# Optimization experiments

Measured on AMD Instinct MI355X. Metric: run time of the kernel, lower is better.

The kernel has to match this reference:

```python
import jax, jax.numpy as jnp
import numpy as np

N_NODES = 10000
N_EDGES = 160000
HID = 128
N_LAYERS = 6
N_RBF = 50
CUTOFF = 10.0
EDGE_IN = 2 * HID + N_RBF + 1  # 307


def setup_inputs() -> dict:
    key = jax.random.key(0)
    ks = jax.random.split(key, 24)
    s = 0.05
    inp = {
        'atomic_numbers': jax.random.randint(ks[0], (N_NODES,), 0, 100),
        'coords': jax.random.normal(ks[1], (N_NODES, 3), jnp.float32),
        'edge_index': jax.random.randint(ks[2], (2, N_EDGES), 0, N_NODES),
        'embed': jax.random.normal(ks[3], (100, HID), jnp.float32) * s,
        # message_net (stacked over layers)
        'mw1': jax.random.normal(ks[4], (N_LAYERS, EDGE_IN, HID), jnp.float32) * s,
        'mb1': jnp.zeros((N_LAYERS, HID), jnp.float32),
        'mw2': jax.random.normal(ks[5], (N_LAYERS, HID, HID), jnp.float32) * s,
        'mb2': jnp.zeros((N_LAYERS, HID), jnp.float32),
        # coord_net
        'cw1': jax.random.normal(ks[6], (N_LAYERS, HID, HID), jnp.float32) * s,
        'cb1': jnp.zeros((N_LAYERS, HID), jnp.float32),
        'cw2': jax.random.normal(ks[7], (N_LAYERS, HID, 1), jnp.float32) * s,
        'cb2': jnp.zeros((N_LAYERS, 1), jnp.float32),
        # feature_net
        'fw': jax.random.normal(ks[8], (N_LAYERS, 2 * HID, HID), jnp.float32) * s,
        'fb': jnp.zeros((N_LAYERS, HID), jnp.float32),
        # energy_predictor
        'ew1': jax.random.normal(ks[9], (HID, HID), jnp.float32) * s,
        'eb1': jnp.zeros((HID,), jnp.float32),
        'ew2': jax.random.normal(ks[10], (HID, 1), jnp.float32) * s,
        'eb2': jnp.zeros((1,), jnp.float32),
    }
    return inp


def _forward(atomic_numbers, coords, edge_index, embed,
             mw1, mb1, mw2, mb2, cw1, cb1, cw2, cb2, fw, fb,
             ew1, eb1, ew2, eb2):
    silu = jax.nn.silu
    n = coords.shape[0]
    row, col = edge_index[0], edge_index[1]
    feats = embed[atomic_numbers]                    # [N, H]
    # RBF edge attributes (computed once from initial coords)
    d = jnp.linalg.norm(coords[row] - coords[col], axis=-1)[:, None]  # [E,1]
    centers = jnp.linspace(0.0, CUTOFF, N_RBF)
    width = CUTOFF / N_RBF
    rbf = jnp.exp(-((d - centers) ** 2) / width)
    cut = 0.5 * (jnp.cos(jnp.pi * d / CUTOFF) + 1.0) * (d < CUTOFF).astype(d.dtype)
    edge_attr = rbf * cut                            # [E, 50]
    for l in range(N_LAYERS):
        diff = coords[row] - coords[col]             # [E, 3]
        edist = jnp.sum(diff * diff, axis=-1, keepdims=True)  # squared dist, [E,1]
        ef = jnp.concatenate([feats[row], feats[col], edist, edge_attr], axis=-1)
        m = silu(silu(ef @ mw1[l] + mb1[l]) @ mw2[l] + mb2[l])        # [E, H]
        w = silu(m @ cw1[l] + cb1[l]) @ cw2[l] + cb2[l]               # [E, 1]
        coords = coords.at[row].add(w * diff)                         # equivariant coord update
        agg = jax.ops.segment_sum(m, row, num_segments=n)             # [N, H]
        feats = silu(jnp.concatenate([feats, agg], axis=-1) @ fw[l] + fb[l])
    atom_e = silu(feats @ ew1 + eb1) @ ew2 + eb2     # [N, 1]
    return jnp.sum(atom_e)


def reference(atomic_numbers, coords, edge_index, embed,
              mw1, mb1, mw2, mb2, cw1, cb1, cw2, cb2, fw, fb,
              ew1, eb1, ew2, eb2):
    return _forward(atomic_numbers, coords, edge_index, embed,
                    mw1, mb1, mw2, mb2, cw1, cb1, cw2, cb2, fw, fb,
                    ew1, eb1, ew2, eb2)
```

## Files before the change

### kernel.cpp

```cpp
#include <hip/hip_runtime.h>
#include <hip/hip_bf16.h>
#include <math.h>

#define N_NODES  10000
#define N_EDGES  160000
#define HID      128
#define N_LAYERS 6
#define N_RBF    50
#define EDGE_IN  307
#define M_TILE   64
#define N_TILES  (N_EDGES / M_TILE)

typedef short bf16x8 __attribute__((ext_vector_type(8)));
typedef float f32x4  __attribute__((ext_vector_type(4)));

__device__ __forceinline__ float silu_f(float x) {
    float e = __expf(-x);
    return x * __builtin_amdgcn_rcpf(1.0f + e);
}
__device__ __forceinline__ short f2bf(float f) {
    union { float f; unsigned u; } v; v.f = f;
    unsigned r = v.u + 0x7FFFu + ((v.u >> 16) & 1u);
    return (short)(r >> 16);
}
__device__ __forceinline__ float bf2f(unsigned short s) {
    union { float f; unsigned u; } v; v.u = ((unsigned)s) << 16;
    return v.f;
}
__device__ __forceinline__ unsigned pk_bf(float a, float b) {
    __hip_bfloat162 h = __float22bfloat162_rn(float2{a, b});
    unsigned u; __builtin_memcpy(&u, &h, 4); return u;
}


__global__ void init_feats_kernel(const int* __restrict__ an,
                                  const float* __restrict__ embed,
                                  short* __restrict__ featsB) {
    int idx = blockIdx.x * blockDim.x + threadIdx.x;
    if (idx < N_NODES * HID) {
        int i = idx >> 7, j = idx & 127;
        featsB[idx] = f2bf(embed[an[i] * HID + j]);
    }
}

__global__ void hist_kernel(const int* __restrict__ row, int* __restrict__ cnt) {
    int e = blockIdx.x * blockDim.x + threadIdx.x;
    if (e < N_EDGES) atomicAdd(&cnt[row[e]], 1);
}

__global__ void scan_kernel(const int* __restrict__ cnt, int* __restrict__ cursor) {
    __shared__ int buf[256];
    __shared__ int carry;
    int tid = threadIdx.x;
    if (tid == 0) carry = 0;
    __syncthreads();
    for (int base = 0; base < N_NODES; base += 256) {
        int v = (base + tid < N_NODES) ? cnt[base + tid] : 0;
        buf[tid] = v;
        __syncthreads();
        for (int off = 1; off < 256; off <<= 1) {
            int x = (tid >= off) ? buf[tid - off] : 0;
            __syncthreads();
            buf[tid] += x;
            __syncthreads();
        }
        int excl = buf[tid] - v + carry;
        if (base + tid < N_NODES) cursor[base + tid] = excl;
        int tot = buf[255];
        __syncthreads();
        if (tid == 0) carry += tot;
        __syncthreads();
    }
}

__global__ void scatter_kernel(const int* __restrict__ row, int* __restrict__ cursor,
                               int* __restrict__ sorted) {
    int e = blockIdx.x * blockDim.x + threadIdx.x;
    if (e < N_EDGES) {
        int p = atomicAdd(&cursor[row[e]], 1);
        sorted[p] = e;
    }
}

__global__ void edgegeom_kernel(const int* __restrict__ sorted,
                                const int* __restrict__ erow, const int* __restrict__ ecol,
                                const float* __restrict__ coords,
                                float* __restrict__ d0, float* __restrict__ cut0) {
    int p = blockIdx.x * 256 + threadIdx.x;
    if (p < N_EDGES) {
        int e = sorted[p];
        int r = erow[e], c = ecol[e];
        float dx = coords[3*r]   - coords[3*c];
        float dy = coords[3*r+1] - coords[3*c+1];
        float dz = coords[3*r+2] - coords[3*c+2];
        float d = sqrtf(dx*dx + dy*dy + dz*dz);
        d0[p] = d;
        cut0[p] = (d < 10.0f) ? 0.5f * (__cosf(0.31415926535f * d) + 1.0f) : 0.0f;
    }
}

#define SZ_M1E 8192
#define SZ_P   32768
#define SZ_M2  16384
#define SZ_C1  16384
#define SZ_F   32768
#define WT_L   (SZ_M1E + SZ_P + SZ_M2 + SZ_C1 + SZ_F)
__global__ void wtrans_kernel(const float* __restrict__ mw1, const float* __restrict__ mw2,
                              const float* __restrict__ cw1, const float* __restrict__ fw,
                              short* __restrict__ wtm1e, short* __restrict__ wtp,
                              short* __restrict__ wtm2, short* __restrict__ wtc1,
                              short* __restrict__ wtf) {
    int idx = blockIdx.x * blockDim.x + threadIdx.x;
    if (idx >= N_LAYERS * WT_L) return;
    int l = idx / WT_L;
    int r = idx - l * WT_L;
    const float* m1 = mw1 + (size_t)l * EDGE_IN * HID;
    if (r < SZ_M1E) {
        int n = r >> 6, k = r & 63;
        float v = 0.f;
        if (k == 0) v = m1[(size_t)256 * HID + n];
        else if (k <= 50) v = m1[(size_t)(256 + k) * HID + n];
        wtm1e[(size_t)l * SZ_M1E + r] = f2bf(v);
    } else if ((r -= SZ_M1E) < SZ_P) {
        int n = r >> 7, k = r & 127;
        float v = (n < HID) ? m1[(size_t)k * HID + n]
                            : m1[(size_t)(HID + k) * HID + (n - HID)];
        wtp[(size_t)l * SZ_P + r] = f2bf(v);
    } else if ((r -= SZ_P) < SZ_M2) {
        int n = r >> 7, k = r & 127;
        wtm2[(size_t)l * SZ_M2 + r] = f2bf(mw2[(size_t)l * HID * HID + (size_t)k * HID + n]);
    } else if ((r -= SZ_M2) < SZ_C1) {
        int n = r >> 7, k = r & 127;
        wtc1[(size_t)l * SZ_C1 + r] = f2bf(cw1[(size_t)l * HID * HID + (size_t)k * HID + n]);
    } else {
        r -= SZ_C1;
        int n = r >> 8, k = r & 255;
        wtf[(size_t)l * SZ_F + r] = f2bf(fw[(size_t)l * 2 * HID * HID + (size_t)k * HID + n]);
    }
}

__global__ __launch_bounds__(256) void p_kernel(
    const short* __restrict__ featsB, const short* __restrict__ wtp,
    short* __restrict__ Pg)
{
    __shared__ short sA[32][136];
    const int tid = threadIdx.x;
    const int n0 = blockIdx.x * 32;
    const int wave = tid >> 6, lane = tid & 63, quad = lane >> 4, lm = lane & 15;

    {
        int el = tid >> 3, kq = (tid & 7) * 16;
        int node = n0 + el;
        if (node < N_NODES) {
            const bf16x8* src = (const bf16x8*)&featsB[(size_t)node * HID + kq];
            *(bf16x8*)&sA[el][kq]     = src[0];
            *(bf16x8*)&sA[el][kq + 8] = src[1];
        } else {
            *(bf16x8*)&sA[el][kq]     = (bf16x8)0;
            *(bf16x8*)&sA[el][kq + 8] = (bf16x8)0;
        }
    }
    bf16x8 bw[4][4];
    #pragma unroll
    for (int h = 0; h < 4; ++h)
        #pragma unroll
        for (int nb = 0; nb < 4; ++nb) {
            int col = wave * 64 + nb * 16 + lm;
            bw[h][nb] = *(const bf16x8*)&wtp[(size_t)col * HID + h * 32 + quad * 8];
        }
    __syncthreads();

    f32x4 acc[2][4];
    #pragma unroll
    for (int mt = 0; mt < 2; ++mt)
        #pragma unroll
        for (int nb = 0; nb < 4; ++nb) acc[mt][nb] = (f32x4)0.f;

    #pragma unroll
    for (int h = 0; h < 4; ++h) {
        bf16x8 af[2];
        af[0] = *(bf16x8*)&sA[lm][h * 32 + quad * 8];
        af[1] = *(bf16x8*)&sA[16 + lm][h * 32 + quad * 8];
        #pragma unroll
        for (int nb = 0; nb < 4; ++nb) {
            acc[0][nb] = __builtin_amdgcn_mfma_f32_16x16x32_bf16(af[0], bw[h][nb], acc[0][nb], 0, 0, 0);
            acc[1][nb] = __builtin_amdgcn_mfma_f32_16x16x32_bf16(af[1], bw[h][nb], acc[1][nb], 0, 0, 0);
        }
    }
    #pragma unroll
    for (int mt = 0; mt < 2; ++mt)
        #pragma unroll
        for (int r = 0; r < 4; ++r) {
            int node = n0 + mt * 16 + quad * 4 + r;
            if (node < N_NODES) {
                #pragma unroll
                for (int nb = 0; nb < 4; ++nb) {
                    int col = wave * 64 + nb * 16 + lm;
                    Pg[(size_t)node * 256 + col] = f2bf(acc[mt][nb][r]);
                }
            }
        }
}


__global__ __launch_bounds__(256) void edge_kernel(
    const int* __restrict__ sorted,
    const int* __restrict__ erow, const int* __restrict__ ecol,
    const float* __restrict__ coords, float* __restrict__ coords_next,
    const short* __restrict__ Pg,
    const float* __restrict__ d0g, const float* __restrict__ cut0g,
    const short* __restrict__ wtm1e, const float* __restrict__ mb1,
    const short* __restrict__ wtm2, const float* __restrict__ mb2,
    const short* __restrict__ wtc1, const float* __restrict__ cb1,
    const float* __restrict__ cw2, const float* __restrict__ cb2,
    float* __restrict__ agg)
{
    __shared__ short sH[M_TILE][136];
    __shared__ short sA[M_TILE][72];
    __shared__ int   srow[M_TILE];
    __shared__ float sdiff[M_TILE][3];
    __shared__ float sW[M_TILE];
    __shared__ float sWp[M_TILE][4];

    const int tid = threadIdx.x;
    const int p0 = blockIdx.x * M_TILE;
    const int wave = tid >> 6, lane = tid & 63, quad = lane >> 4, lm = lane & 15;
    const int colA = wave * 32 + lm, colB = colA + 16;
    const int el = tid >> 2, sub = tid & 3;

    int e = sorted[p0 + el];
    int r = erow[e], c = ecol[e];
    float dx = coords[3*r]   - coords[3*c];
    float dy = coords[3*r+1] - coords[3*c+1];
    float dz = coords[3*r+2] - coords[3*c+2];
    float ds2 = dx*dx + dy*dy + dz*dz;
    if (sub == 0) {
        srow[el] = r;
        sdiff[el][0] = dx; sdiff[el][1] = dy; sdiff[el][2] = dz;
    }
    float b1A = mb1[colA], b1B = mb1[colB];
    float b2A = mb2[colA], b2B = mb2[colB];
    float c1A = cb1[colA], c1B = cb1[colB];
    float vA  = cw2[colA], vB  = cw2[colB];
    const float cb2v = cb2[0];

    {
        int kq = sub * 32;
        const short* p1 = &Pg[(size_t)r * 256 + kq];
        const short* p2 = &Pg[(size_t)c * 256 + 128 + kq];
        #pragma unroll
        for (int g = 0; g < 4; ++g) {
            bf16x8 a = *(const bf16x8*)&p1[g * 8];
            bf16x8 b = *(const bf16x8*)&p2[g * 8];
            bf16x8 o;
            #pragma unroll
            for (int j = 0; j < 8; j += 2) {
                float s0 = bf2f((unsigned short)a[j])     + bf2f((unsigned short)b[j]);
                float s1 = bf2f((unsigned short)a[j + 1]) + bf2f((unsigned short)b[j + 1]);
                unsigned u = pk_bf(s0, s1);
                o[j] = (short)(u & 0xFFFF); o[j + 1] = (short)(u >> 16);
            }
            *(bf16x8*)&sH[el][kq + g * 8] = o;
        }
    }
    {
        float dv = d0g[p0 + el], ct = cut0g[p0 + el];
        int kq = sub * 16;
        #pragma unroll
        for (int g = 0; g < 2; ++g) {
            bf16x8 v;
            #pragma unroll
            for (int j = 0; j < 8; ++j) {
                int k = kq + g * 8 + j;
                float val = 0.f;
                if (k == 0) val = ds2;
                else if (k <= N_RBF) {
                    float cen = (float)(k - 1) * (10.0f / 49.0f);
                    float t = dv - cen;
                    val = __expf(-t * t * 5.0f) * ct;
                }
                v[j] = f2bf(val);
            }
            *(bf16x8*)&sA[el][kq + g * 8] = v;
        }
    }
    bf16x8 bw1[2][2];
    #pragma unroll
    for (int h = 0; h < 2; ++h) {
        bw1[h][0] = *(const bf16x8*)&wtm1e[(size_t)colA * 64 + h * 32 + quad * 8];
        bw1[h][1] = *(const bf16x8*)&wtm1e[(size_t)colB * 64 + h * 32 + quad * 8];
    }
    bf16x8 bw2[4][2];
    #pragma unroll
    for (int ks = 0; ks < 4; ++ks) {
        bw2[ks][0] = *(const bf16x8*)&wtm2[(size_t)colA * HID + ks * 32 + quad * 8];
        bw2[ks][1] = *(const bf16x8*)&wtm2[(size_t)colB * HID + ks * 32 + quad * 8];
    }
    __syncthreads();

    f32x4 acc[4][2];
    #pragma unroll
    for (int mt = 0; mt < 4; ++mt) { acc[mt][0] = (f32x4)0.f; acc[mt][1] = (f32x4)0.f; }

    #pragma unroll
    for (int h = 0; h < 2; ++h) {
        bf16x8 af[4];
        #pragma unroll
        for (int mt = 0; mt < 4; ++mt)
            af[mt] = *(bf16x8*)&sA[mt * 16 + lm][h * 32 + quad * 8];
        #pragma unroll
        for (int nb = 0; nb < 2; ++nb)
            #pragma unroll
            for (int mt = 0; mt < 4; ++mt)
                acc[mt][nb] = __builtin_amdgcn_mfma_f32_16x16x32_bf16(
                    af[mt], bw1[h][nb], acc[mt][nb], 0, 0, 0);
    }
    #pragma unroll
    for (int mt = 0; mt < 4; ++mt) {
        #pragma unroll
        for (int r2 = 0; r2 < 4; ++r2) {
            int row = mt * 16 + quad * 4 + r2;
            float pA = bf2f((unsigned short)sH[row][colA]);
            float pB = bf2f((unsigned short)sH[row][colB]);
            float hA = silu_f(acc[mt][0][r2] + pA + b1A);
            float hB = silu_f(acc[mt][1][r2] + pB + b1B);
            unsigned u = pk_bf(hA, hB);
            sH[row][colA] = (short)(u & 0xFFFF);
            sH[row][colB] = (short)(u >> 16);
        }
        acc[mt][0] = (f32x4)0.f; acc[mt][1] = (f32x4)0.f;
    }
    __syncthreads();

    #pragma unroll
    for (int ks = 0; ks < 4; ++ks) {
        bf16x8 af[4];
        #pragma unroll
        for (int mt = 0; mt < 4; ++mt)
            af[mt] = *(bf16x8*)&sH[mt * 16 + lm][ks * 32 + quad * 8];
        #pragma unroll
        for (int nb = 0; nb < 2; ++nb)
            #pragma unroll
            for (int mt = 0; mt < 4; ++mt)
                acc[mt][nb] = __builtin_amdgcn_mfma_f32_16x16x32_bf16(
                    af[mt], bw2[ks][nb], acc[mt][nb], 0, 0, 0);
    }
    bf16x8 bw3[4][2];
    #pragma unroll
    for (int ks = 0; ks < 4; ++ks) {
        bw3[ks][0] = *(const bf16x8*)&wtc1[(size_t)colA * HID + ks * 32 + quad * 8];
        bw3[ks][1] = *(const bf16x8*)&wtc1[(size_t)colB * HID + ks * 32 + quad * 8];
    }
    __syncthreads();
    #pragma unroll
    for (int nb = 0; nb < 2; ++nb) {
        int col = wave * 32 + nb * 16 + lm;
        float b = nb ? b2B : b2A;
        #pragma unroll
        for (int mt = 0; mt < 4; ++mt) {
            float g = 0.f;
            #pragma unroll
            for (int r2 = 0; r2 < 4; ++r2) {
                int row = mt * 16 + quad * 4 + r2;
                float mv = silu_f(acc[mt][nb][r2] + b);
                sH[row][col] = f2bf(mv);
                g += mv;
                if (r2 == 3 || srow[row + 1] != srow[row]) {
                    atomicAdd(&agg[(size_t)srow[row] * HID + col], g);
                    g = 0.f;
                }
            }
            acc[mt][nb] = (f32x4)0.f;
        }
    }
    __syncthreads();

    #pragma unroll
    for (int ks = 0; ks < 4; ++ks) {
        bf16x8 af[4];
        #pragma unroll
        for (int mt = 0; mt < 4; ++mt)
            af[mt] = *(bf16x8*)&sH[mt * 16 + lm][ks * 32 + quad * 8];
        #pragma unroll
        for (int nb = 0; nb < 2; ++nb)
            #pragma unroll
            for (int mt = 0; mt < 4; ++mt)
                acc[mt][nb] = __builtin_amdgcn_mfma_f32_16x16x32_bf16(
                    af[mt], bw3[ks][nb], acc[mt][nb], 0, 0, 0);
    }
    {
        float wp[4][4];
        #pragma unroll
        for (int mt = 0; mt < 4; ++mt)
            #pragma unroll
            for (int r2 = 0; r2 < 4; ++r2) wp[mt][r2] = 0.f;
        #pragma unroll
        for (int nb = 0; nb < 2; ++nb) {
            float b = nb ? c1B : c1A;
            float vv = nb ? vB : vA;
            #pragma unroll
            for (int mt = 0; mt < 4; ++mt)
                #pragma unroll
                for (int r2 = 0; r2 < 4; ++r2)
                    wp[mt][r2] += silu_f(acc[mt][nb][r2] + b) * vv;
        }
        #pragma unroll
        for (int mt = 0; mt < 4; ++mt)
            #pragma unroll
            for (int r2 = 0; r2 < 4; ++r2) {
                float v = wp[mt][r2];
                v += __shfl_xor(v, 1); v += __shfl_xor(v, 2);
                v += __shfl_xor(v, 4); v += __shfl_xor(v, 8);
                if (lm == 0) sWp[mt * 16 + quad * 4 + r2][wave] = v;
            }
    }
    __syncthreads();
    if (tid < M_TILE)
        sW[tid] = cb2v + sWp[tid][0] + sWp[tid][1] + sWp[tid][2] + sWp[tid][3];
    __syncthreads();
    if (tid < M_TILE) {
        bool leader = (tid == 0) || (srow[tid] != srow[tid - 1]);
        if (leader) {
            int rr = srow[tid];
            float ax = 0.f, ay = 0.f, az = 0.f;
            for (int k = tid; k < M_TILE && srow[k] == rr; ++k) {
                ax += sW[k] * sdiff[k][0];
                ay += sW[k] * sdiff[k][1];
                az += sW[k] * sdiff[k][2];
            }
            atomicAdd(&coords_next[3*rr+0], ax);
            atomicAdd(&coords_next[3*rr+1], ay);
            atomicAdd(&coords_next[3*rr+2], az);
        }
    }
}

__global__ __launch_bounds__(256) void node_kernel(
    const short* __restrict__ featsB, float* __restrict__ agg,
    const short* __restrict__ wtf, const float* __restrict__ fb,
    short* __restrict__ outB,
    const short* __restrict__ wtp_next, short* __restrict__ Pg,
    const float* __restrict__ csrc, float* __restrict__ cdst)
{
    __shared__ short sA[32][72];
    __shared__ short sO[32][136];

    const int tid = threadIdx.x;
    const int n0 = blockIdx.x * 32;
    const int wave = tid >> 6, lane = tid & 63, quad = lane >> 4, lm = lane & 15;

    {
        int idx = blockIdx.x * 256 + tid;
        if (idx < 3 * N_NODES) cdst[idx] = csrc[idx];
    }
    float fbA = fb[wave * 32 + lm], fbB = fb[wave * 32 + 16 + lm];

    f32x4 acc[2][2];
    acc[0][0] = (f32x4)0.f; acc[0][1] = (f32x4)0.f;
    acc[1][0] = (f32x4)0.f; acc[1][1] = (f32x4)0.f;

    for (int c = 0; c < 4; ++c) {
        int k0 = c * 64;
        bf16x8 bw[2][2];
        #pragma unroll
        for (int h = 0; h < 2; ++h) {
            int col0 = wave * 32 + lm;
            bw[h][0] = *(const bf16x8*)&wtf[(size_t)col0 * 256 + k0 + h * 32 + quad * 8];
            bw[h][1] = *(const bf16x8*)&wtf[(size_t)(col0 + 16) * 256 + k0 + h * 32 + quad * 8];
        }
        {
            int el = tid >> 3, kq = (tid & 7) * 8;
            int node = n0 + el;
            if (node < N_NODES) {
                if (c < 2) {
                    *(bf16x8*)&sA[el][kq] =
                        *(const bf16x8*)&featsB[(size_t)node * HID + k0 + kq];
                } else {
                    float* ap = &agg[(size_t)node * HID + (k0 - 128) + kq];
                    bf16x8 v;
                    #pragma unroll
                    for (int j = 0; j < 8; j += 2) {
                        unsigned u = pk_bf(ap[j], ap[j + 1]);
                        v[j] = (short)(u & 0xFFFF); v[j + 1] = (short)(u >> 16);
                    }
                    *(bf16x8*)&sA[el][kq] = v;
                    *(float4*)&ap[0] = make_float4(0.f, 0.f, 0.f, 0.f);
                    *(float4*)&ap[4] = make_float4(0.f, 0.f, 0.f, 0.f);
                }
            } else {
                *(bf16x8*)&sA[el][kq] = (bf16x8)0;
            }
        }
        __syncthreads();
        #pragma unroll
        for (int h = 0; h < 2; ++h) {
            bf16x8 af[2];
            af[0] = *(bf16x8*)&sA[lm][h * 32 + quad * 8];
            af[1] = *(bf16x8*)&sA[16 + lm][h * 32 + quad * 8];
            #pragma unroll
            for (int nb = 0; nb < 2; ++nb) {
                acc[0][nb] = __builtin_amdgcn_mfma_f32_16x16x32_bf16(af[0], bw[h][nb], acc[0][nb], 0, 0, 0);
                acc[1][nb] = __builtin_amdgcn_mfma_f32_16x16x32_bf16(af[1], bw[h][nb], acc[1][nb], 0, 0, 0);
            }
        }
        __syncthreads();
    }
    bf16x8 bwp[4][4];
    if (wtp_next) {
        #pragma unroll
        for (int ks = 0; ks < 4; ++ks)
            #pragma unroll
            for (int nb = 0; nb < 4; ++nb) {
                int col = wave * 64 + nb * 16 + lm;
                bwp[ks][nb] = *(const bf16x8*)&wtp_next[(size_t)col * HID + ks * 32 + quad * 8];
            }
    }
    #pragma unroll
    for (int mt = 0; mt < 2; ++mt) {
        #pragma unroll
        for (int r = 0; r < 4; ++r) {
            int row = mt * 16 + quad * 4 + r;
            float hA = silu_f(acc[mt][0][r] + fbA);
            float hB = silu_f(acc[mt][1][r] + fbB);
            unsigned u = pk_bf(hA, hB);
            sO[row][wave * 32 + lm]      = (short)(u & 0xFFFF);
            sO[row][wave * 32 + 16 + lm] = (short)(u >> 16);
        }
    }
    __syncthreads();
    {
        int row = tid >> 3, ch = (tid & 7) * 8;
        int node = n0 + row;
        if (node < N_NODES) {
            *(bf16x8*)&outB[(size_t)node * HID + ch]      = *(bf16x8*)&sO[row][ch];
            *(bf16x8*)&outB[(size_t)node * HID + 64 + ch] = *(bf16x8*)&sO[row][64 + ch];
        }
    }
    if (wtp_next) {
        f32x4 ap2[2][4];
        #pragma unroll
        for (int mt = 0; mt < 2; ++mt)
            #pragma unroll
            for (int nb = 0; nb < 4; ++nb) ap2[mt][nb] = (f32x4)0.f;
        #pragma unroll
        for (int ks = 0; ks < 4; ++ks) {
            bf16x8 af[2];
            af[0] = *(bf16x8*)&sO[lm][ks * 32 + quad * 8];
            af[1] = *(bf16x8*)&sO[16 + lm][ks * 32 + quad * 8];
            #pragma unroll
            for (int nb = 0; nb < 4; ++nb) {
                ap2[0][nb] = __builtin_amdgcn_mfma_f32_16x16x32_bf16(af[0], bwp[ks][nb], ap2[0][nb], 0, 0, 0);
                ap2[1][nb] = __builtin_amdgcn_mfma_f32_16x16x32_bf16(af[1], bwp[ks][nb], ap2[1][nb], 0, 0, 0);
            }
        }
        #pragma unroll
        for (int mt = 0; mt < 2; ++mt)
            #pragma unroll
            for (int r = 0; r < 4; ++r) {
                int node = n0 + mt * 16 + quad * 4 + r;
                if (node < N_NODES) {
                    #pragma unroll
                    for (int nb = 0; nb < 4; ++nb) {
                        int col = wave * 64 + nb * 16 + lm;
                        Pg[(size_t)node * 256 + col] = f2bf(ap2[mt][nb][r]);
                    }
                }
            }
    }
}

#define FMA8(r, aq) \
    acc[r][0] += (aq)*b0.x; acc[r][1] += (aq)*b0.y; acc[r][2] += (aq)*b0.z; acc[r][3] += (aq)*b0.w; \
    acc[r][4] += (aq)*b1.x; acc[r][5] += (aq)*b1.y; acc[r][6] += (aq)*b1.z; acc[r][7] += (aq)*b1.w;

__global__ __launch_bounds__(256) void energy_kernel(
    const short* __restrict__ featsB,
    const float* __restrict__ ew1, const float* __restrict__ eb1,
    const float* __restrict__ ew2, const float* __restrict__ eb2,
    float* __restrict__ out)
{
    __shared__ float sA[64][20];
    __shared__ float sB[16][HID];
    __shared__ float sV[HID];
    __shared__ float red[256];
    int tid = threadIdx.x;
    int n0 = blockIdx.x * 64;
    const int tr = tid >> 4, tc = tid & 15;
    const int r0 = tr * 4, c0 = tc * 4, c1 = c0 + 64;
    const int el = tid >> 2, kq = (tid & 3) * 4;

    if (tid < HID) sV[tid] = ew2[tid];

    float acc[4][8];
    #pragma unroll
    for (int i = 0; i < 4; i++)
        #pragma unroll
        for (int j = 0; j < 8; j++) acc[i][j] = 0.f;

    for (int kt = 0; kt < 8; ++kt) {
        int k0 = kt * 16;
        {
            int k = k0 + kq;
            int node = n0 + el;
            float4 v = make_float4(0,0,0,0);
            if (node < N_NODES) {
                const unsigned short* p = (const unsigned short*)&featsB[(size_t)node * HID + k];
                v.x = bf2f(p[0]); v.y = bf2f(p[1]); v.z = bf2f(p[2]); v.w = bf2f(p[3]);
            }
            *(float4*)&sA[el][kq] = v;
        }
        {
            int bk = tid >> 4, bj = (tid & 15) * 8;
            int k = k0 + bk;
            *(float4*)&sB[bk][bj]     = *(const float4*)&ew1[(size_t)k * HID + bj];
            *(float4*)&sB[bk][bj + 4] = *(const float4*)&ew1[(size_t)k * HID + bj + 4];
        }
        __syncthreads();
        #pragma unroll
        for (int kk4 = 0; kk4 < 4; ++kk4) {
            float4 a0 = *(const float4*)&sA[r0 + 0][kk4 * 4];
            float4 a1 = *(const float4*)&sA[r0 + 1][kk4 * 4];
            float4 a2 = *(const float4*)&sA[r0 + 2][kk4 * 4];
            float4 a3 = *(const float4*)&sA[r0 + 3][kk4 * 4];
            #pragma unroll
            for (int q = 0; q < 4; ++q) {
                int kk = kk4 * 4 + q;
                float4 b0 = *(const float4*)&sB[kk][c0];
                float4 b1 = *(const float4*)&sB[kk][c1];
                float q0 = ((const float*)&a0)[q], q1 = ((const float*)&a1)[q];
                float q2 = ((const float*)&a2)[q], q3 = ((const float*)&a3)[q];
                FMA8(0, q0) FMA8(1, q1) FMA8(2, q2) FMA8(3, q3)
            }
        }
        __syncthreads();
    }
    float part = 0.f;
    #pragma unroll
    for (int i = 0; i < 4; i++) {
        int node = n0 + r0 + i;
        if (node < N_NODES) {
            #pragma unroll
            for (int j = 0; j < 4; j++) {
                part += silu_f(acc[i][j]     + eb1[c0+j]) * sV[c0+j];
                part += silu_f(acc[i][4 + j] + eb1[c1+j]) * sV[c1+j];
            }
        }
    }
    red[tid] = part;
    __syncthreads();
    for (int s = 128; s > 0; s >>= 1) {
        if (tid < s) red[tid] += red[tid + s];
        __syncthreads();
    }
    if (tid == 0) {
        float v = red[0];
        if (blockIdx.x == 0) v += eb2[0] * (float)N_NODES;
        atomicAdd(out, v);
    }
}


extern "C" void kernel_launch(void* const* d_in, const int* in_sizes, int n_in,
                              void* d_out, int out_size, void* d_ws, size_t ws_size,
                              hipStream_t stream)
{
    const int*   an     = (const int*)  d_in[0];
    const float* coords = (const float*)d_in[1];
    const int*   ei     = (const int*)  d_in[2];
    const float* embed  = (const float*)d_in[3];
    const float* mw1 = (const float*)d_in[4];
    const float* mb1 = (const float*)d_in[5];
    const float* mw2 = (const float*)d_in[6];
    const float* mb2 = (const float*)d_in[7];
    const float* cw1 = (const float*)d_in[8];
    const float* cb1 = (const float*)d_in[9];
    const float* cw2 = (const float*)d_in[10];
    const float* cb2 = (const float*)d_in[11];
    const float* fw  = (const float*)d_in[12];
    const float* fb  = (const float*)d_in[13];
    const float* ew1 = (const float*)d_in[14];
    const float* eb1 = (const float*)d_in[15];
    const float* ew2 = (const float*)d_in[16];
    const float* eb2 = (const float*)d_in[17];
    float* out = (float*)d_out;

    char* w = (char*)d_ws;
    size_t off = 0;
    auto alloc = [&](size_t bytes) -> char* {
        char* p = w + off;
        off = (off + bytes + 511) & ~(size_t)511;
        return p;
    };
    short* featsB0 = (short*)alloc((size_t)N_NODES * HID * 2);
    short* featsB1 = (short*)alloc((size_t)N_NODES * HID * 2);
    short* Pg      = (short*)alloc((size_t)N_NODES * 256 * 2);
    float* agg     = (float*)alloc((size_t)N_NODES * HID * 4);
    float* cA      = (float*)alloc((size_t)N_NODES * 3 * 4);
    float* cB      = (float*)alloc((size_t)N_NODES * 3 * 4);
    float* d0      = (float*)alloc((size_t)N_EDGES * 4);
    float* cut0    = (float*)alloc((size_t)N_EDGES * 4);
    int*   sorted  = (int*)  alloc((size_t)N_EDGES * 4);
    int*   cnt     = (int*)  alloc((size_t)N_NODES * 4);
    int*   cursor  = (int*)  alloc((size_t)N_NODES * 4);
    short* wtm1e   = (short*)alloc((size_t)N_LAYERS * SZ_M1E * 2);
    short* wtp     = (short*)alloc((size_t)N_LAYERS * SZ_P * 2);
    short* wtm2    = (short*)alloc((size_t)N_LAYERS * SZ_M2 * 2);
    short* wtc1    = (short*)alloc((size_t)N_LAYERS * SZ_C1 * 2);
    short* wtf     = (short*)alloc((size_t)N_LAYERS * SZ_F * 2);

    const int* erow = ei;
    const int* ecol = ei + N_EDGES;

    hipMemsetAsync(cnt, 0, (size_t)N_NODES * 4, stream);
    hipMemsetAsync(agg, 0, (size_t)N_NODES * HID * 4, stream);
    init_feats_kernel<<<(N_NODES * HID + 255) / 256, 256, 0, stream>>>(an, embed, featsB0);
    wtrans_kernel<<<(N_LAYERS * WT_L + 255) / 256, 256, 0, stream>>>(
        mw1, mw2, cw1, fw, wtm1e, wtp, wtm2, wtc1, wtf);
    hipMemcpyAsync(cA, coords, (size_t)N_NODES * 3 * 4, hipMemcpyDeviceToDevice, stream);
    hipMemcpyAsync(cB, coords, (size_t)N_NODES * 3 * 4, hipMemcpyDeviceToDevice, stream);
    hist_kernel<<<(N_EDGES + 255) / 256, 256, 0, stream>>>(erow, cnt);
    scan_kernel<<<1, 256, 0, stream>>>(cnt, cursor);
    scatter_kernel<<<(N_EDGES + 255) / 256, 256, 0, stream>>>(erow, cursor, sorted);
    edgegeom_kernel<<<N_EDGES / 256, 256, 0, stream>>>(sorted, erow, ecol, cA, d0, cut0);
    p_kernel<<<(N_NODES + 31) / 32, 256, 0, stream>>>(featsB0, wtp, Pg);

    short* fc = featsB0; short* fn = featsB1;
    float* cc = cA;      float* cn = cB;
    for (int l = 0; l < N_LAYERS; ++l) {
        edge_kernel<<<N_TILES, 256, 0, stream>>>(
            sorted, erow, ecol, cc, cn, Pg, d0, cut0,
            wtm1e + (size_t)l * SZ_M1E, mb1 + (size_t)l * HID,
            wtm2  + (size_t)l * SZ_M2,  mb2 + (size_t)l * HID,
            wtc1  + (size_t)l * SZ_C1,  cb1 + (size_t)l * HID,
            cw2 + (size_t)l * HID,      cb2 + l, agg);
        node_kernel<<<(N_NODES + 31) / 32, 256, 0, stream>>>(
            fc, agg, wtf + (size_t)l * SZ_F, fb + (size_t)l * HID, fn,
            (l + 1 < N_LAYERS) ? (wtp + (size_t)(l + 1) * SZ_P) : (const short*)nullptr,
            Pg, cn, cc);
        { short* t = fc; fc = fn; fn = t; }
        { float* t = cc; cc = cn; cn = t; }
    }
    hipMemsetAsync(out, 0, 4, stream);
    energy_kernel<<<(N_NODES + 63) / 64, 256, 0, stream>>>(fc, ew1, eb1, ew2, eb2, out);
}
```

Baseline: 711.4 us.

## Use 8-wave edge blocks and 16-node node-kernel tiles

The edge kernel moves from 256 to 512 threads per 64-edge tile, so each wave owns 16 output columns instead of 32. Staging, MFMA, segmented atomic aggregation and the coord-net reduction are reworked to match, with eight partial sums per edge. The node kernel processes 16 nodes per block with K chunks of 128 instead of 32 nodes with K chunks of 64, doubling its grid and dropping the bounds checks. The aim is more waves in flight and shorter per-wave dependency chains, at the cost of more blocks, repeated weight loads per block and heavier register and LDS pressure from larger blocks.

```diff
diff --git a/kernel.cpp b/kernel.cpp
--- a/kernel.cpp
+++ b/kernel.cpp
@@ -10,6 +10,7 @@
 #define EDGE_IN  307
 #define M_TILE   64
 #define N_TILES  (N_EDGES / M_TILE)
+#define EB       512
 
 typedef short bf16x8 __attribute__((ext_vector_type(8)));
 typedef float f32x4  __attribute__((ext_vector_type(4)));
@@ -203,7 +204,7 @@
 }
 
 
-__global__ __launch_bounds__(256) void edge_kernel(
+__global__ __launch_bounds__(EB) void edge_kernel(
     const int* __restrict__ sorted,
     const int* __restrict__ erow, const int* __restrict__ ecol,
     const float* __restrict__ coords, float* __restrict__ coords_next,
@@ -220,13 +221,13 @@
     __shared__ int   srow[M_TILE];
     __shared__ float sdiff[M_TILE][3];
     __shared__ float sW[M_TILE];
-    __shared__ float sWp[M_TILE][4];
+    __shared__ float sWp[M_TILE][8];
 
     const int tid = threadIdx.x;
     const int p0 = blockIdx.x * M_TILE;
     const int wave = tid >> 6, lane = tid & 63, quad = lane >> 4, lm = lane & 15;
-    const int colA = wave * 32 + lm, colB = colA + 16;
-    const int el = tid >> 2, sub = tid & 3;
+    const int colA = wave * 16 + lm;
+    const int el = tid >> 3, sub = tid & 7;
 
     int e = sorted[p0 + el];
     int r = erow[e], c = ecol[e];
@@ -238,18 +239,16 @@
         srow[el] = r;
         sdiff[el][0] = dx; sdiff[el][1] = dy; sdiff[el][2] = dz;
     }
-    float b1A = mb1[colA], b1B = mb1[colB];
-    float b2A = mb2[colA], b2B = mb2[colB];
-    float c1A = cb1[colA], c1B = cb1[colB];
-    float vA  = cw2[colA], vB  = cw2[colB];
+    float b1A = mb1[colA], b2A = mb2[colA];
+    float c1A = cb1[colA], vA = cw2[colA];
     const float cb2v = cb2[0];
 
     {
-        int kq = sub * 32;
+        int kq = sub * 16;
         const short* p1 = &Pg[(size_t)r * 256 + kq];
         const short* p2 = &Pg[(size_t)c * 256 + 128 + kq];
         #pragma unroll
-        for (int g = 0; g < 4; ++g) {
+        for (int g = 0; g < 2; ++g) {
             bf16x8 a = *(const bf16x8*)&p1[g * 8];
             bf16x8 b = *(const bf16x8*)&p2[g * 8];
             bf16x8 o;
@@ -265,42 +264,35 @@
     }
     {
         float dv = d0g[p0 + el], ct = cut0g[p0 + el];
-        int kq = sub * 16;
-        #pragma unroll
-        for (int g = 0; g < 2; ++g) {
-            bf16x8 v;
-            #pragma unroll
-            for (int j = 0; j < 8; ++j) {
-                int k = kq + g * 8 + j;
-                float val = 0.f;
-                if (k == 0) val = ds2;
-                else if (k <= N_RBF) {
-                    float cen = (float)(k - 1) * (10.0f / 49.0f);
-                    float t = dv - cen;
-                    val = __expf(-t * t * 5.0f) * ct;
-                }
-                v[j] = f2bf(val);
-            }
-            *(bf16x8*)&sA[el][kq + g * 8] = v;
-        }
-    }
-    bf16x8 bw1[2][2];
-    #pragma unroll
-    for (int h = 0; h < 2; ++h) {
-        bw1[h][0] = *(const bf16x8*)&wtm1e[(size_t)colA * 64 + h * 32 + quad * 8];
-        bw1[h][1] = *(const bf16x8*)&wtm1e[(size_t)colB * 64 + h * 32 + quad * 8];
-    }
-    bf16x8 bw2[4][2];
-    #pragma unroll
-    for (int ks = 0; ks < 4; ++ks) {
-        bw2[ks][0] = *(const bf16x8*)&wtm2[(size_t)colA * HID + ks * 32 + quad * 8];
-        bw2[ks][1] = *(const bf16x8*)&wtm2[(size_t)colB * HID + ks * 32 + quad * 8];
-    }
-    __syncthreads();
-
-    f32x4 acc[4][2];
-    #pragma unroll
-    for (int mt = 0; mt < 4; ++mt) { acc[mt][0] = (f32x4)0.f; acc[mt][1] = (f32x4)0.f; }
+        int kq = sub * 8;
+        bf16x8 v;
+        #pragma unroll
+        for (int j = 0; j < 8; ++j) {
+            int k = kq + j;
+            float val = 0.f;
+            if (k == 0) val = ds2;
+            else if (k <= N_RBF) {
+                float cen = (float)(k - 1) * (10.0f / 49.0f);
+                float t = dv - cen;
+                val = __expf(-t * t * 5.0f) * ct;
+            }
+            v[j] = f2bf(val);
+        }
+        *(bf16x8*)&sA[el][kq] = v;
+    }
+    bf16x8 bw1[2];
+    #pragma unroll
+    for (int h = 0; h < 2; ++h)
+        bw1[h] = *(const bf16x8*)&wtm1e[(size_t)colA * 64 + h * 32 + quad * 8];
+    bf16x8 bw2[4];
+    #pragma unroll
+    for (int ks = 0; ks < 4; ++ks)
+        bw2[ks] = *(const bf16x8*)&wtm2[(size_t)colA * HID + ks * 32 + quad * 8];
+    __syncthreads();
+
+    f32x4 acc[4];
+    #pragma unroll
+    for (int mt = 0; mt < 4; ++mt) acc[mt] = (f32x4)0.f;
 
     #pragma unroll
     for (int h = 0; h < 2; ++h) {
@@ -309,26 +301,23 @@
         for (int mt = 0; mt < 4; ++mt)
             af[mt] = *(bf16x8*)&sA[mt * 16 + lm][h * 32 + quad * 8];
         #pragma unroll
-        for (int nb = 0; nb < 2; ++nb)
-            #pragma unroll
-            for (int mt = 0; mt < 4; ++mt)
-                acc[mt][nb] = __builtin_amdgcn_mfma_f32_16x16x32_bf16(
-                    af[mt], bw1[h][nb], acc[mt][nb], 0, 0, 0);
+        for (int mt = 0; mt < 4; ++mt)
+            acc[mt] = __builtin_amdgcn_mfma_f32_16x16x32_bf16(af[mt], bw1[h], acc[mt], 0, 0, 0);
     }
     #pragma unroll
     for (int mt = 0; mt < 4; ++mt) {
         #pragma unroll
-        for (int r2 = 0; r2 < 4; ++r2) {
-            int row = mt * 16 + quad * 4 + r2;
-            float pA = bf2f((unsigned short)sH[row][colA]);
-            float pB = bf2f((unsigned short)sH[row][colB]);
-            float hA = silu_f(acc[mt][0][r2] + pA + b1A);
-            float hB = silu_f(acc[mt][1][r2] + pB + b1B);
-            unsigned u = pk_bf(hA, hB);
-            sH[row][colA] = (short)(u & 0xFFFF);
-            sH[row][colB] = (short)(u >> 16);
-        }
-        acc[mt][0] = (f32x4)0.f; acc[mt][1] = (f32x4)0.f;
+        for (int r2 = 0; r2 < 4; r2 += 2) {
+            int row0 = mt * 16 + quad * 4 + r2;
+            float pA0 = bf2f((unsigned short)sH[row0][colA]);
+            float pA1 = bf2f((unsigned short)sH[row0 + 1][colA]);
+            float h0 = silu_f(acc[mt][r2]     + pA0 + b1A);
+            float h1 = silu_f(acc[mt][r2 + 1] + pA1 + b1A);
+            unsigned u = pk_bf(h0, h1);
+            sH[row0][colA]     = (short)(u & 0xFFFF);
+            sH[row0 + 1][colA] = (short)(u >> 16);
+        }
+        acc[mt] = (f32x4)0.f;
     }
     __syncthreads();
 
@@ -339,39 +328,35 @@
         for (int mt = 0; mt < 4; ++mt)
             af[mt] = *(bf16x8*)&sH[mt * 16 + lm][ks * 32 + quad * 8];
         #pragma unroll
-        for (int nb = 0; nb < 2; ++nb)
-            #pragma unroll
-            for (int mt = 0; mt < 4; ++mt)
-                acc[mt][nb] = __builtin_amdgcn_mfma_f32_16x16x32_bf16(
-                    af[mt], bw2[ks][nb], acc[mt][nb], 0, 0, 0);
-    }
-    bf16x8 bw3[4][2];
-    #pragma unroll
-    for (int ks = 0; ks < 4; ++ks) {
-        bw3[ks][0] = *(const bf16x8*)&wtc1[(size_t)colA * HID + ks * 32 + quad * 8];
-        bw3[ks][1] = *(const bf16x8*)&wtc1[(size_t)colB * HID + ks * 32 + quad * 8];
-    }
-    __syncthreads();
-    #pragma unroll
-    for (int nb = 0; nb < 2; ++nb) {
-        int col = wave * 32 + nb * 16 + lm;
-        float b = nb ? b2B : b2A;
-        #pragma unroll
-        for (int mt = 0; mt < 4; ++mt) {
-            float g = 0.f;
-            #pragma unroll
-            for (int r2 = 0; r2 < 4; ++r2) {
-                int row = mt * 16 + quad * 4 + r2;
-                float mv = silu_f(acc[mt][nb][r2] + b);
-                sH[row][col] = f2bf(mv);
-                g += mv;
-                if (r2 == 3 || srow[row + 1] != srow[row]) {
-                    atomicAdd(&agg[(size_t)srow[row] * HID + col], g);
-                    g = 0.f;
-                }
-            }
-            acc[mt][nb] = (f32x4)0.f;
-        }
+        for (int mt = 0; mt < 4; ++mt)
+            acc[mt] = __builtin_amdgcn_mfma_f32_16x16x32_bf16(af[mt], bw2[ks], acc[mt], 0, 0, 0);
+    }
+    bf16x8 bw3[4];
+    #pragma unroll
+    for (int ks = 0; ks < 4; ++ks)
+        bw3[ks] = *(const bf16x8*)&wtc1[(size_t)colA * HID + ks * 32 + quad * 8];
+    __syncthreads();
+    #pragma unroll
+    for (int mt = 0; mt < 4; ++mt) {
+        int row0 = mt * 16 + quad * 4;
+        float m0 = silu_f(acc[mt][0] + b2A);
+        float m1 = silu_f(acc[mt][1] + b2A);
+        float m2 = silu_f(acc[mt][2] + b2A);
+        float m3 = silu_f(acc[mt][3] + b2A);
+        unsigned u01 = pk_bf(m0, m1), u23 = pk_bf(m2, m3);
+        sH[row0][colA]     = (short)(u01 & 0xFFFF);
+        sH[row0 + 1][colA] = (short)(u01 >> 16);
+        sH[row0 + 2][colA] = (short)(u23 & 0xFFFF);
+        sH[row0 + 3][colA] = (short)(u23 >> 16);
+        float g = m0;
+        if (srow[row0 + 1] != srow[row0]) { atomicAdd(&agg[(size_t)srow[row0] * HID + colA], g); g = 0.f; }
+        g += m1;
+        if (srow[row0 + 2] != srow[row0 + 1]) { atomicAdd(&agg[(size_t)srow[row0 + 1] * HID + colA], g); g = 0.f; }
+        g += m2;
+        if (srow[row0 + 3] != srow[row0 + 2]) { atomicAdd(&agg[(size_t)srow[row0 + 2] * HID + colA], g); g = 0.f; }
+        g += m3;
+        atomicAdd(&agg[(size_t)srow[row0 + 3] * HID + colA], g);
+        acc[mt] = (f32x4)0.f;
     }
     __syncthreads();
 
@@ -382,41 +367,26 @@
         for (int mt = 0; mt < 4; ++mt)
             af[mt] = *(bf16x8*)&sH[mt * 16 + lm][ks * 32 + quad * 8];
         #pragma unroll
-        for (int nb = 0; nb < 2; ++nb)
-            #pragma unroll
-            for (int mt = 0; mt < 4; ++mt)
-                acc[mt][nb] = __builtin_amdgcn_mfma_f32_16x16x32_bf16(
-                    af[mt], bw3[ks][nb], acc[mt][nb], 0, 0, 0);
-    }
-    {
-        float wp[4][4];
-        #pragma unroll
         for (int mt = 0; mt < 4; ++mt)
-            #pragma unroll
-            for (int r2 = 0; r2 < 4; ++r2) wp[mt][r2] = 0.f;
-        #pragma unroll
-        for (int nb = 0; nb < 2; ++nb) {
-            float b = nb ? c1B : c1A;
-            float vv = nb ? vB : vA;
-            #pragma unroll
-            for (int mt = 0; mt < 4; ++mt)
-                #pragma unroll
-                for (int r2 = 0; r2 < 4; ++r2)
-                    wp[mt][r2] += silu_f(acc[mt][nb][r2] + b) * vv;
-        }
-        #pragma unroll
-        for (int mt = 0; mt < 4; ++mt)
-            #pragma unroll
-            for (int r2 = 0; r2 < 4; ++r2) {
-                float v = wp[mt][r2];
-                v += __shfl_xor(v, 1); v += __shfl_xor(v, 2);
-                v += __shfl_xor(v, 4); v += __shfl_xor(v, 8);
-                if (lm == 0) sWp[mt * 16 + quad * 4 + r2][wave] = v;
-            }
-    }
-    __syncthreads();
-    if (tid < M_TILE)
-        sW[tid] = cb2v + sWp[tid][0] + sWp[tid][1] + sWp[tid][2] + sWp[tid][3];
+            acc[mt] = __builtin_amdgcn_mfma_f32_16x16x32_bf16(af[mt], bw3[ks], acc[mt], 0, 0, 0);
+    }
+    #pragma unroll
+    for (int mt = 0; mt < 4; ++mt) {
+        #pragma unroll
+        for (int r2 = 0; r2 < 4; ++r2) {
+            float v = silu_f(acc[mt][r2] + c1A) * vA;
+            v += __shfl_xor(v, 1); v += __shfl_xor(v, 2);
+            v += __shfl_xor(v, 4); v += __shfl_xor(v, 8);
+            if (lm == 0) sWp[mt * 16 + quad * 4 + r2][wave] = v;
+        }
+    }
+    __syncthreads();
+    if (tid < M_TILE) {
+        float s = cb2v;
+        #pragma unroll
+        for (int w = 0; w < 8; ++w) s += sWp[tid][w];
+        sW[tid] = s;
+    }
     __syncthreads();
     if (tid < M_TILE) {
         bool leader = (tid == 0) || (srow[tid] != srow[tid - 1]);
@@ -442,11 +412,11 @@
     const short* __restrict__ wtp_next, short* __restrict__ Pg,
     const float* __restrict__ csrc, float* __restrict__ cdst)
 {
-    __shared__ short sA[32][72];
-    __shared__ short sO[32][136];
+    __shared__ short sA[16][136];
+    __shared__ short sO[16][136];
 
     const int tid = threadIdx.x;
-    const int n0 = blockIdx.x * 32;
+    const int n0 = blockIdx.x * 16;
     const int wave = tid >> 6, lane = tid & 63, quad = lane >> 4, lm = lane & 15;
 
     {
@@ -455,53 +425,43 @@
     }
     float fbA = fb[wave * 32 + lm], fbB = fb[wave * 32 + 16 + lm];
 
-    f32x4 acc[2][2];
-    acc[0][0] = (f32x4)0.f; acc[0][1] = (f32x4)0.f;
-    acc[1][0] = (f32x4)0.f; acc[1][1] = (f32x4)0.f;
-
-    for (int c = 0; c < 4; ++c) {
-        int k0 = c * 64;
-        bf16x8 bw[2][2];
-        #pragma unroll
-        for (int h = 0; h < 2; ++h) {
+    f32x4 acc[2];
+    acc[0] = (f32x4)0.f; acc[1] = (f32x4)0.f;
+
+    for (int ch = 0; ch < 2; ++ch) {
+        int k0 = ch * 128;
+        bf16x8 bw[4][2];
+        #pragma unroll
+        for (int ks = 0; ks < 4; ++ks) {
             int col0 = wave * 32 + lm;
-            bw[h][0] = *(const bf16x8*)&wtf[(size_t)col0 * 256 + k0 + h * 32 + quad * 8];
-            bw[h][1] = *(const bf16x8*)&wtf[(size_t)(col0 + 16) * 256 + k0 + h * 32 + quad * 8];
+            bw[ks][0] = *(const bf16x8*)&wtf[(size_t)col0 * 256 + k0 + ks * 32 + quad * 8];
+            bw[ks][1] = *(const bf16x8*)&wtf[(size_t)(col0 + 16) * 256 + k0 + ks * 32 + quad * 8];
         }
         {
-            int el = tid >> 3, kq = (tid & 7) * 8;
+            int el = tid >> 4, kq = (tid & 15) * 8;
             int node = n0 + el;
-            if (node < N_NODES) {
-                if (c < 2) {
-                    *(bf16x8*)&sA[el][kq] =
-                        *(const bf16x8*)&featsB[(size_t)node * HID + k0 + kq];
-                } else {
-                    float* ap = &agg[(size_t)node * HID + (k0 - 128) + kq];
-                    bf16x8 v;
-                    #pragma unroll
-                    for (int j = 0; j < 8; j += 2) {
-                        unsigned u = pk_bf(ap[j], ap[j + 1]);
-                        v[j] = (short)(u & 0xFFFF); v[j + 1] = (short)(u >> 16);
-                    }
-                    *(bf16x8*)&sA[el][kq] = v;
-                    *(float4*)&ap[0] = make_float4(0.f, 0.f, 0.f, 0.f);
-                    *(float4*)&ap[4] = make_float4(0.f, 0.f, 0.f, 0.f);
+            if (ch == 0) {
+                *(bf16x8*)&sA[el][kq] =
+                    *(const bf16x8*)&featsB[(size_t)node * HID + kq];
+            } else {
+                float* ap = &agg[(size_t)node * HID + kq];
+                bf16x8 v;
+                #pragma unroll
+                for (int j = 0; j < 8; j += 2) {
+                    unsigned u = pk_bf(ap[j], ap[j + 1]);
+                    v[j] = (short)(u & 0xFFFF); v[j + 1] = (short)(u >> 16);
                 }
-            } else {
-                *(bf16x8*)&sA[el][kq] = (bf16x8)0;
-            }
-        }
-        __syncthreads();
-        #pragma unroll
-        for (int h = 0; h < 2; ++h) {
-            bf16x8 af[2];
-            af[0] = *(bf16x8*)&sA[lm][h * 32 + quad * 8];
-            af[1] = *(bf16x8*)&sA[16 + lm][h * 32 + quad * 8];
-            #pragma unroll
-            for (int nb = 0; nb < 2; ++nb) {
-                acc[0][nb] = __builtin_amdgcn_mfma_f32_16x16x32_bf16(af[0], bw[h][nb], acc[0][nb], 0, 0, 0);
-                acc[1][nb] = __builtin_amdgcn_mfma_f32_16x16x32_bf16(af[1], bw[h][nb], acc[1][nb], 0, 0, 0);
-            }
+                *(bf16x8*)&sA[el][kq] = v;
+                *(float4*)&ap[0] = make_float4(0.f, 0.f, 0.f, 0.f);
+                *(float4*)&ap[4] = make_float4(0.f, 0.f, 0.f, 0.f);
+            }
+        }
+        __syncthreads();
+        #pragma unroll
+        for (int ks = 0; ks < 4; ++ks) {
+            bf16x8 af = *(bf16x8*)&sA[lm][ks * 32 + quad * 8];
+            acc[0] = __builtin_amdgcn_mfma_f32_16x16x32_bf16(af, bw[ks][0], acc[0], 0, 0, 0);
+            acc[1] = __builtin_amdgcn_mfma_f32_16x16x32_bf16(af, bw[ks][1], acc[1], 0, 0, 0);
         }
         __syncthreads();
     }
@@ -516,56 +476,40 @@
             }
     }
     #pragma unroll
-    for (int mt = 0; mt < 2; ++mt) {
+    for (int r = 0; r < 4; ++r) {
+        int row = quad * 4 + r;
+        float hA = silu_f(acc[0][r] + fbA);
+        float hB = silu_f(acc[1][r] + fbB);
+        unsigned u = pk_bf(hA, hB);
+        sO[row][wave * 32 + lm]      = (short)(u & 0xFFFF);
+        sO[row][wave * 32 + 16 + lm] = (short)(u >> 16);
+    }
+    __syncthreads();
+    {
+        int row = tid >> 4, ch2 = (tid & 15) * 8;
+        int node = n0 + row;
+        *(bf16x8*)&outB[(size_t)node * HID + ch2] = *(bf16x8*)&sO[row][ch2];
+    }
+    if (wtp_next) {
+        f32x4 ap2[4];
+        #pragma unroll
+        for (int nb = 0; nb < 4; ++nb) ap2[nb] = (f32x4)0.f;
+        #pragma unroll
+        for (int ks = 0; ks < 4; ++ks) {
+            bf16x8 af = *(bf16x8*)&sO[lm][ks * 32 + quad * 8];
+            #pragma unroll
+            for (int nb = 0; nb < 4; ++nb)
+                ap2[nb] = __builtin_amdgcn_mfma_f32_16x16x32_bf16(af, bwp[ks][nb], ap2[nb], 0, 0, 0);
+        }
         #pragma unroll
         for (int r = 0; r < 4; ++r) {
-            int row = mt * 16 + quad * 4 + r;
-            float hA = silu_f(acc[mt][0][r] + fbA);
-            float hB = silu_f(acc[mt][1][r] + fbB);
-            unsigned u = pk_bf(hA, hB);
-            sO[row][wave * 32 + lm]      = (short)(u & 0xFFFF);
-            sO[row][wave * 32 + 16 + lm] = (short)(u >> 16);
-        }
-    }
-    __syncthreads();
-    {
-        int row = tid >> 3, ch = (tid & 7) * 8;
-        int node = n0 + row;
-        if (node < N_NODES) {
-            *(bf16x8*)&outB[(size_t)node * HID + ch]      = *(bf16x8*)&sO[row][ch];
-            *(bf16x8*)&outB[(size_t)node * HID + 64 + ch] = *(bf16x8*)&sO[row][64 + ch];
-        }
-    }
-    if (wtp_next) {
-        f32x4 ap2[2][4];
-        #pragma unroll
-        for (int mt = 0; mt < 2; ++mt)
-            #pragma unroll
-            for (int nb = 0; nb < 4; ++nb) ap2[mt][nb] = (f32x4)0.f;
-        #pragma unroll
-        for (int ks = 0; ks < 4; ++ks) {
-            bf16x8 af[2];
-            af[0] = *(bf16x8*)&sO[lm][ks * 32 + quad * 8];
-            af[1] = *(bf16x8*)&sO[16 + lm][ks * 32 + quad * 8];
+            int node = n0 + quad * 4 + r;
             #pragma unroll
             for (int nb = 0; nb < 4; ++nb) {
-                ap2[0][nb] = __builtin_amdgcn_mfma_f32_16x16x32_bf16(af[0], bwp[ks][nb], ap2[0][nb], 0, 0, 0);
-                ap2[1][nb] = __builtin_amdgcn_mfma_f32_16x16x32_bf16(af[1], bwp[ks][nb], ap2[1][nb], 0, 0, 0);
-            }
-        }
-        #pragma unroll
-        for (int mt = 0; mt < 2; ++mt)
-            #pragma unroll
-            for (int r = 0; r < 4; ++r) {
-                int node = n0 + mt * 16 + quad * 4 + r;
-                if (node < N_NODES) {
-                    #pragma unroll
-                    for (int nb = 0; nb < 4; ++nb) {
-                        int col = wave * 64 + nb * 16 + lm;
-                        Pg[(size_t)node * 256 + col] = f2bf(ap2[mt][nb][r]);
-                    }
-                }
-            }
+                int col = wave * 64 + nb * 16 + lm;
+                Pg[(size_t)node * 256 + col] = f2bf(ap2[nb][r]);
+            }
+        }
     }
 }
 
@@ -727,13 +671,13 @@
     short* fc = featsB0; short* fn = featsB1;
     float* cc = cA;      float* cn = cB;
     for (int l = 0; l < N_LAYERS; ++l) {
-        edge_kernel<<<N_TILES, 256, 0, stream>>>(
+        edge_kernel<<<N_TILES, EB, 0, stream>>>(
             sorted, erow, ecol, cc, cn, Pg, d0, cut0,
             wtm1e + (size_t)l * SZ_M1E, mb1 + (size_t)l * HID,
             wtm2  + (size_t)l * SZ_M2,  mb2 + (size_t)l * HID,
             wtc1  + (size_t)l * SZ_C1,  cb1 + (size_t)l * HID,
             cw2 + (size_t)l * HID,      cb2 + l, agg);
-        node_kernel<<<(N_NODES + 31) / 32, 256, 0, stream>>>(
+        node_kernel<<<N_NODES / 16, 256, 0, stream>>>(
             fc, agg, wtf + (size_t)l * SZ_F, fb + (size_t)l * HID, fn,
             (l + 1 < N_LAYERS) ? (wtp + (size_t)(l + 1) * SZ_P) : (const short*)nullptr,
             Pg, cn, cc);
```

Result: slower. 737.0 us (+3.6%).
